# Optimization experiments

Measured on AMD Instinct MI355X. Metric: run time of the kernel, lower is better.

## Reference

```python
import jax, jax.numpy as jnp
import numpy as np

N_BUILDINGS = 4096
NUM_CLUSTERS = 128
EMBED_DIM = 128
TEMPORAL_DIM = 24


def setup_inputs() -> dict:
    key = jax.random.key(0)
    ks = jax.random.split(key, 12)
    E, N, C, T = EMBED_DIM, N_BUILDINGS, NUM_CLUSTERS, TEMPORAL_DIM

    def lin(k, fi, fo):
        k1, k2 = jax.random.split(k)
        w = jax.random.normal(k1, (fo, fi), jnp.float32) / np.sqrt(fi).astype(np.float32)
        b = jax.random.normal(k2, (fo,), jnp.float32) * 0.01
        return w, b

    fp_w1, fp_b1 = lin(ks[0], 2 * E + 2, 128)
    fp_w2, fp_b2 = lin(ks[1], 128, 64)
    fp_w3, fp_b3 = lin(ks[2], 64, 1)
    en_w1, en_b1 = lin(ks[3], 1, 16)
    en_w2, en_b2 = lin(ks[4], 16, 1)
    ps_w1, ps_b1 = lin(ks[5], E, 32)
    ps_w2, ps_b2 = lin(ks[6], 32, 1)

    embeddings = jax.random.normal(ks[7], (1, N, E), jnp.float32)
    generation = jax.random.uniform(ks[8], (1, N, T), jnp.float32) * 50.0
    consumption = jax.random.uniform(ks[9], (1, N, T), jnp.float32) * 50.0
    positions = jax.random.uniform(ks[10], (1, N, 2), jnp.float32) * 1000.0
    cluster_assignments = (jnp.arange(N) % C)[None, :].astype(jnp.int32)

    return dict(embeddings=embeddings, generation=generation, consumption=consumption,
                positions=positions,
                fp_w1=fp_w1, fp_b1=fp_b1, fp_w2=fp_w2, fp_b2=fp_b2, fp_w3=fp_w3, fp_b3=fp_b3,
                en_w1=en_w1, en_b1=en_b1, en_w2=en_w2, en_b2=en_b2,
                ps_w1=ps_w1, ps_b1=ps_b1, ps_w2=ps_w2, ps_b2=ps_b2,
                cluster_assignments=cluster_assignments, num_clusters=C, current_hour=12)


def _greedy_cluster(net0, prio, effm, pf):
    """Greedy allocation within one cluster. net0,prio: [K]; effm,pf: [K,K].
    Surplus rows and deficit cols are both visited in descending priority order;
    non-surplus rows have avail=0 and non-deficit cols have needed<=0, matching the
    original code's subset selection + break/continue semantics."""
    K = net0.shape[0]
    order = jnp.argsort(-prio)
    inv = jnp.argsort(order)
    net_o = net0[order]
    eff_o = effm[order][:, order]
    pf_o = pf[order][:, order]

    def outer(dnet, i):
        avail0 = jnp.maximum(net_o[i], 0.0)  # surplus net is never mutated

        def inner(carry, j):
            avail, dn = carry
            needed = -dn[j]
            active = (avail > 0.0) & (needed > 0.0)
            f = jnp.where(active, jnp.minimum(jnp.minimum(avail, needed), pf_o[i, j]), 0.0)
            dn = dn.at[j].add(f * eff_o[i, j])  # deficit receives delivered flow
            return (avail - f, dn), (f, active)

        (_, dnet), (frow, arow) = jax.lax.scan(inner, (avail0, dnet), jnp.arange(K))
        return dnet, (frow, arow)

    dnet, (flows_o, act_o) = jax.lax.scan(outer, net_o, jnp.arange(K))
    return flows_o[inv][:, inv], act_o[inv][:, inv], dnet[inv]


def _forward(embeddings, generation, consumption, positions,
             fp_w1, fp_b1, fp_w2, fp_b2, fp_w3, fp_b3,
             en_w1, en_b1, en_w2, en_b2,
             ps_w1, ps_b1, ps_w2, ps_b2,
             cluster_assignments, num_clusters, current_hour):
    B, N, E = embeddings.shape
    C = num_clusters
    K = N // C
    net = generation[0, :, current_hour] - consumption[0, :, current_hour]  # [N]

    g = jnp.argsort(cluster_assignments[0]).reshape(C, K)  # [C,K] building ids per cluster
    emb_c = embeddings[0][g]   # [C,K,E]
    pos_c = positions[0][g]    # [C,K,2]
    net_c = net[g]             # [C,K]

    # priority scorer (eval mode)
    h = jax.nn.relu(emb_c @ ps_w1.T + ps_b1)
    prio_c = jax.nn.sigmoid(h @ ps_w2.T + ps_b2)[..., 0]  # [C,K]

    # pairwise distances within cluster
    dist = jnp.linalg.norm(pos_c[:, :, None, :] - pos_c[:, None, :, :], axis=-1)  # [C,K,K]

    # efficiency net: eff = 0.85 + 0.13*sigmoid(MLP(dist/1000))
    eh = jax.nn.relu((dist / 1000.0)[..., None] * en_w1[:, 0] + en_b1)  # [C,K,K,16]
    eff = 0.85 + 0.13 * jax.nn.sigmoid(eh @ en_w2.T + en_b2)[..., 0]    # [C,K,K]

    # flow predictor on concat([emb_i, emb_j, dist, hour/24]); split W1 to avoid
    # materializing the [C,K,K,2E+2] feature tensor. Dropout is eval-mode identity.
    W1a, W1b = fp_w1[:, :E], fp_w1[:, E:2 * E]
    w1d, w1h = fp_w1[:, 2 * E], fp_w1[:, 2 * E + 1]
    hi = emb_c @ W1a.T  # [C,K,128]
    hj = emb_c @ W1b.T  # [C,K,128]
    hour_f = current_hour / 24.0
    h1 = jax.nn.relu(hi[:, :, None, :] + hj[:, None, :, :] + dist[..., None] * w1d + hour_f * w1h + fp_b1)
    h2 = jax.nn.relu(h1 @ fp_w2.T + fp_b2)
    pflow = jax.nn.softplus(h2 @ fp_w3.T + fp_b3)[..., 0]  # [C,K,K]

    flows_c, act_c, dnet_c = jax.vmap(_greedy_cluster)(net_c, prio_c, eff, pflow)

    sharing = jnp.zeros((N, N), embeddings.dtype).at[g[:, :, None], g[:, None, :]].set(flows_c)
    effmat = jnp.ones((N, N), embeddings.dtype).at[g[:, :, None], g[:, None, :]].set(
        jnp.where(act_c, eff, 1.0))
    net_after = jnp.zeros((N,), embeddings.dtype).at[g].set(dnet_c)

    sharing = sharing[None]
    effmat = effmat[None]
    total_shared = sharing.sum()
    energy_sent = sharing.sum(axis=2)
    energy_received = (sharing * effmat).sum(axis=1)
    return sharing, effmat, total_shared, energy_sent, energy_received, net_after[None]


def reference(embeddings, generation, consumption, positions,
              fp_w1, fp_b1, fp_w2, fp_b2, fp_w3, fp_b3,
              en_w1, en_b1, en_w2, en_b2,
              ps_w1, ps_b1, ps_w2, ps_b2,
              cluster_assignments, num_clusters, current_hour):
    return _forward(embeddings, generation, consumption, positions,
                    fp_w1, fp_b1, fp_w2, fp_b2, fp_w3, fp_b3,
                    en_w1, en_b1, en_w2, en_b2,
                    ps_w1, ps_b1, ps_w2, ps_b2,
                    cluster_assignments, num_clusters, current_hour)
```

## Files before the change

### kernel.cpp

```cpp
#include <hip/hip_runtime.h>
#include <math.h>

#define NB 4096
#define NC 128
#define NK 32
#define NE 128

typedef __bf16 bf16x8 __attribute__((ext_vector_type(8)));
typedef float floatx4 __attribute__((ext_vector_type(4)));

__device__ __forceinline__ float sigmoidf_(float x){
  if (x >= 0.f){ float z = expf(-x); return 1.f/(1.f+z); }
  float z = expf(x); return z/(1.f+z);
}
__device__ __forceinline__ float softplusf_(float x){
  return fmaxf(x, 0.f) + log1pf(expf(-fabsf(x)));
}
__device__ __forceinline__ unsigned int pack_bf16(float a, float b){
  unsigned short ua = __builtin_bit_cast(unsigned short, (__bf16)a);
  unsigned short ub = __builtin_bit_cast(unsigned short, (__bf16)b);
  return (unsigned int)ua | ((unsigned int)ub << 16);
}

__global__ void k_hijprio(const float* __restrict__ emb, const float* __restrict__ gen,
                          const float* __restrict__ cons, const float* __restrict__ fp_w1,
                          const float* __restrict__ fp_b1, const float* __restrict__ fp_w2,
                          const float* __restrict__ ps_w1, const float* __restrict__ ps_b1,
                          const float* __restrict__ ps_w2, const float* __restrict__ ps_b2,
                          const int* __restrict__ assign, const int* __restrict__ hourp,
                          float* __restrict__ hi, float* __restrict__ hj,
                          float* __restrict__ net, float* __restrict__ prio,
                          int* __restrict__ g, int* __restrict__ row_of,
                          float* __restrict__ w1d_c, float* __restrict__ bzc,
                          uint4* __restrict__ w2f, float* __restrict__ total){
  int bid = blockIdx.x;
  int t = threadIdx.x;
  if (bid < 512){
    __shared__ float es[8*132];
    __shared__ float wsm[32*132];
    __shared__ float wa_s[128*36];
    __shared__ float wb_s[128*36];
    int i0 = bid*8;
    for (int idx = t; idx < 8*128; idx += 256){
      int b = idx >> 7, e = idx & 127;
      es[b*132 + e] = emb[(i0 + b)*128 + e];
    }
    for (int idx = t; idx < 4096; idx += 256){
      int q = idx >> 7, e = idx & 127;
      wsm[q*132 + e] = ps_w1[q*128 + e];
    }
    int o = t & 127, half = t >> 7;
    float ai[4], aj[4];
#pragma unroll
    for (int r = 0; r < 4; ++r){ ai[r] = 0.f; aj[r] = 0.f; }
    for (int ch = 0; ch < 4; ++ch){
      int ec = ch << 5;
      if (ch) __syncthreads();
      for (int idx = t; idx < 4096; idx += 256){
        int row = idx >> 5, e2 = idx & 31;
        wa_s[row*36 + e2] = fp_w1[row*258 + ec + e2];
        wb_s[row*36 + e2] = fp_w1[row*258 + 128 + ec + e2];
      }
      __syncthreads();
      const float* war = &wa_s[o*36];
      const float* wbr = &wb_s[o*36];
#pragma unroll
      for (int e2 = 0; e2 < 32; e2 += 4){
        float4 wav = *(const float4*)&war[e2];
        float4 wbv = *(const float4*)&wbr[e2];
        float wa0 = wav.x, wa1 = wav.y, wa2 = wav.z, wa3 = wav.w;
        float wb0 = wbv.x, wb1 = wbv.y, wb2 = wbv.z, wb3 = wbv.w;
        int e = ec + e2;
#pragma unroll
        for (int r = 0; r < 4; ++r){
          float4 ev = *(const float4*)&es[(half*4 + r)*132 + e];
          ai[r] = fmaf(ev.x, wa0, fmaf(ev.y, wa1, fmaf(ev.z, wa2, fmaf(ev.w, wa3, ai[r]))));
          aj[r] = fmaf(ev.x, wb0, fmaf(ev.y, wb1, fmaf(ev.z, wb2, fmaf(ev.w, wb3, aj[r]))));
        }
      }
    }
#pragma unroll
    for (int r = 0; r < 4; ++r){
      int b = i0 + half*4 + r;
      hi[b*128 + o] = ai[r];
      hj[b*128 + o] = aj[r];
    }
    {
      int bl = t >> 5, q = t & 31;
      int i = i0 + bl;
      float acc = ps_b1[q];
      const float* er = &es[bl*132];
      const float* wr = &wsm[q*132];
      for (int e = 0; e < 128; e += 4){
        float4 ev = *(const float4*)&er[e];
        float4 wv = *(const float4*)&wr[e];
        acc = fmaf(ev.x, wv.x, acc);
        acc = fmaf(ev.y, wv.y, acc);
        acc = fmaf(ev.z, wv.z, acc);
        acc = fmaf(ev.w, wv.w, acc);
      }
      float v = fmaxf(acc, 0.f) * ps_w2[q];
      for (int m = 16; m >= 1; m >>= 1) v += __shfl_xor(v, m, 32);
      if (q == 0){
        prio[i] = sigmoidf_(v + ps_b2[0]);
        int h = hourp[0];
        net[i] = gen[i*24 + h] - cons[i*24 + h];
      }
    }
  } else if (bid < 528){
    __shared__ int hist[NC];
    __shared__ int loc[256];
    int start = (bid - 512)*256;
    for (int c = t; c < NC; c += 256) hist[c] = 0;
    __syncthreads();
    for (int j = t; j < start; j += 256) atomicAdd(&hist[assign[j]], 1);
    int i = start + t;
    int c = assign[i];
    loc[t] = c;
    __syncthreads();
    int r = hist[c];
    for (int j = 0; j < 256; ++j) r += (j < t && loc[j] == c) ? 1 : 0;
    if (r >= NK) r = NK - 1;
    g[c*NK + r] = i;
    row_of[i] = c*NK + r;
  } else if (bid == 528){
    if (t < 128){
      float hour_f = (float)hourp[0] / 24.0f;
      w1d_c[t] = fp_w1[t*258 + 256];
      bzc[t]   = fmaf(hour_f, fp_w1[t*258 + 257], fp_b1[t]);
    }
    if (t == 128) total[0] = 0.f;
  } else {
    for (int ff = t; ff < 1024; ff += 256){
      int lane = ff & 63, fi = ff >> 6;
      int nt = fi >> 2, ks = fi & 3;
      int o = nt*16 + (lane & 15);
      int kb = ks*32 + (lane >> 4)*8;
      const float* src = fp_w2 + o*128 + kb;
      uint4 u;
      u.x = pack_bf16(src[0], src[1]);
      u.y = pack_bf16(src[2], src[3]);
      u.z = pack_bf16(src[4], src[5]);
      u.w = pack_bf16(src[6], src[7]);
      w2f[ff] = u;
    }
  }
}

__global__ __launch_bounds__(512) void k_pflow(
    const float* __restrict__ hi, const float* __restrict__ hj,
    const float* __restrict__ pos, const float* __restrict__ w1d_c,
    const float* __restrict__ bzc, const uint4* __restrict__ w2f,
    const float* __restrict__ fp_b2, const float* __restrict__ fp_w3,
    const float* __restrict__ fp_b3, const float* __restrict__ en_w1,
    const float* __restrict__ en_b1, const float* __restrict__ en_w2,
    const float* __restrict__ en_b2, const int* __restrict__ g,
    float* __restrict__ pf_g, float* __restrict__ ef_g){
  __shared__ float px[32], py[32];
  __shared__ int gl[32];
  int t = threadIdx.x;
  int lane = t & 63, wv = t >> 6;
  int c = blockIdx.x >> 1, hb = blockIdx.x & 1;
  if (t < 32){
    int b = g[c*NK + t];
    gl[t] = b;
    px[t] = pos[2*b];
    py[t] = pos[2*b + 1];
  }
  __syncthreads();
  {
    int l16 = lane & 15, quad = lane >> 4;
    bf16x8 bfr[4][4];
#pragma unroll
    for (int nt = 0; nt < 4; ++nt)
#pragma unroll
      for (int ks = 0; ks < 4; ++ks)
        bfr[nt][ks] = __builtin_bit_cast(bf16x8, w2f[(nt*4 + ks)*64 + lane]);
    float b2v[4], w3v[4];
#pragma unroll
    for (int nt = 0; nt < 4; ++nt){
      b2v[nt] = fp_b2[nt*16 + l16];
      w3v[nt] = fp_w3[nt*16 + l16];
    }
    float b3 = fp_b3[0];
    const float4* wd4 = (const float4*)w1d_c;
    const float4* bz4 = (const float4*)bzc;
    for (int it = 0; it < 4; ++it){
      int tile = hb*32 + it*8 + wv;
      int i = tile >> 1, j0 = (tile & 1)*16;
      int j = j0 + l16;
      float dx = px[i] - px[j], dy = py[i] - py[j];
      float d = sqrtf(fmaf(dx, dx, dy*dy));
      const float4* hi4 = (const float4*)(hi + gl[i]*128);
      const float4* hj4 = (const float4*)(hj + gl[j]*128);
      bf16x8 af[4];
#pragma unroll
      for (int ks = 0; ks < 4; ++ks){
        int q8 = ks*8 + quad*2;
        float4 a0 = hi4[q8], a1 = hi4[q8 + 1];
        float4 b0 = hj4[q8], b1 = hj4[q8 + 1];
        float4 w0 = wd4[q8], w1 = wd4[q8 + 1];
        float4 z0 = bz4[q8], z1 = bz4[q8 + 1];
        float v0 = fmaxf(a0.x + b0.x + fmaf(d, w0.x, z0.x), 0.f);
        float v1 = fmaxf(a0.y + b0.y + fmaf(d, w0.y, z0.y), 0.f);
        float v2 = fmaxf(a0.z + b0.z + fmaf(d, w0.z, z0.z), 0.f);
        float v3 = fmaxf(a0.w + b0.w + fmaf(d, w0.w, z0.w), 0.f);
        float v4 = fmaxf(a1.x + b1.x + fmaf(d, w1.x, z1.x), 0.f);
        float v5 = fmaxf(a1.y + b1.y + fmaf(d, w1.y, z1.y), 0.f);
        float v6 = fmaxf(a1.z + b1.z + fmaf(d, w1.z, z1.z), 0.f);
        float v7 = fmaxf(a1.w + b1.w + fmaf(d, w1.w, z1.w), 0.f);
        uint4 u;
        u.x = pack_bf16(v0, v1);
        u.y = pack_bf16(v2, v3);
        u.z = pack_bf16(v4, v5);
        u.w = pack_bf16(v6, v7);
        af[ks] = __builtin_bit_cast(bf16x8, u);
      }
      floatx4 acc[4];
#pragma unroll
      for (int nt = 0; nt < 4; ++nt){
        acc[nt] = (floatx4){0.f, 0.f, 0.f, 0.f};
#pragma unroll
        for (int ks = 0; ks < 4; ++ks)
          acc[nt] = __builtin_amdgcn_mfma_f32_16x16x32_bf16(af[ks], bfr[nt][ks], acc[nt], 0, 0, 0);
      }
#pragma unroll
      for (int r = 0; r < 4; ++r){
        float s = 0.f;
#pragma unroll
        for (int nt = 0; nt < 4; ++nt)
          s = fmaf(fmaxf(acc[nt][r] + b2v[nt], 0.f), w3v[nt], s);
#pragma unroll
        for (int m = 8; m >= 1; m >>= 1) s += __shfl_xor(s, m);
        if (l16 == 0)
          pf_g[c*1024 + i*32 + j0 + quad*4 + r] = softplusf_(s + b3);
      }
    }
  }
  {
    int e = hb*512 + t;
    int ii = e >> 5, jj = e & 31;
    float dx = px[ii] - px[jj], dy = py[ii] - py[jj];
    float d = sqrtf(fmaf(dx, dx, dy*dy));
    float ds = d * (1.0f/1000.0f);
    float acc = en_b2[0];
#pragma unroll
    for (int q = 0; q < 16; ++q)
      acc = fmaf(fmaxf(fmaf(ds, en_w1[q], en_b1[q]), 0.f), en_w2[q], acc);
    ef_g[c*1024 + e] = 0.85f + 0.13f*sigmoidf_(acc);
  }
}

__global__ __launch_bounds__(256) void k_greedy(
    const float* __restrict__ net, const float* __restrict__ prio,
    const int* __restrict__ g, const float* __restrict__ pf_g,
    const float* __restrict__ ef_g,
    float* __restrict__ fl_c, float* __restrict__ ef_c, float* __restrict__ total,
    float* __restrict__ esent, float* __restrict__ erecv, float* __restrict__ nafter){
  __shared__ float pf_s[1024];
  __shared__ float ef_s[1024];
  __shared__ float fl_s[1024];
  __shared__ float efa_s[1024];
  __shared__ int gl[32];
  __shared__ int order_s[32];
  int t = threadIdx.x;
  int c = blockIdx.x;
  if (t < 32) gl[t] = g[c*NK + t];
  ((float4*)pf_s)[t] = ((const float4*)(pf_g + c*1024))[t];
  ((float4*)ef_s)[t] = ((const float4*)(ef_g + c*1024))[t];
  __syncthreads();
  if (t < 64){
    int tl = t & 31;
    float pr = (t < 32) ? prio[gl[t]] : -1e30f;
    int rank = 0;
    for (int k = 0; k < 32; ++k){
      float pk = __shfl(pr, k, 32);
      rank += ((pk > pr) || (pk == pr && k < tl)) ? 1 : 0;
    }
    if (t < 32) order_s[rank] = t;
  }
  __syncthreads();
  if (t < 64){
    int tl = t & 31;
    int b = order_s[tl];
    float net0 = net[gl[b]];
    float dnet = net0;
    float recv = 0.f;
    for (int i = 0; i < 32; ++i){
      int a = order_s[i];
      float av0 = fmaxf(__shfl(net0, i, 32), 0.f);
      float pf = pf_s[a*32 + b];
      float ef = ef_s[a*32 + b];
      float needed = -dnet;
      float m = (needed > 0.f) ? fminf(needed, pf) : 0.f;
      float s = m;
#pragma unroll
      for (int dd = 1; dd < 32; dd <<= 1){
        float u = __shfl_up(s, dd, 32);
        if (tl >= dd) s += u;
      }
      float Se = __shfl_up(s, 1, 32);
      if (tl == 0) Se = 0.f;
      float rprev = fmaxf(av0 - Se, 0.f);
      int act = (rprev > 0.f) && (needed > 0.f);
      float f = fminf(m, rprev);
      dnet = fmaf(f, ef, dnet);
      recv = fmaf(f, ef, recv);
      if (t < 32){
        fl_s[a*32 + b]  = f;
        efa_s[a*32 + b] = act ? ef : 1.0f;
      }
    }
    if (t < 32){
      nafter[gl[b]] = dnet;
      erecv[gl[b]]  = recv;
    }
  }
  __syncthreads();
  for (int e = t; e < 1024; e += 256){
    fl_c[c*1024 + e] = fl_s[e];
    ef_c[c*1024 + e] = efa_s[e];
  }
  if (t < 32){
    float rs = 0.f;
#pragma unroll
    for (int j = 0; j < 32; ++j)
      rs += fl_s[t*32 + ((j + t) & 31)];
    esent[gl[t]] = rs;
    float cs = rs;
    for (int m = 16; m >= 1; m >>= 1) cs += __shfl_xor(cs, m, 32);
    if (t == 0) atomicAdd(total, cs);
  }
}

__global__ __launch_bounds__(256) void k_write(
    const float* __restrict__ fl_c, const float* __restrict__ ef_c,
    const int* __restrict__ g, const int* __restrict__ row_of,
    float* __restrict__ sharing, float* __restrict__ effm){
  __shared__ float rowS[4096];
  __shared__ float rowE[4096];
  __shared__ int   cols[32];
  __shared__ float vals[32];
  __shared__ float vale[32];
  int t = threadIdx.x;
  int r = blockIdx.x;
  int ra = row_of[r];
  int c = ra >> 5, a = ra & 31;
  if (t < 32){
    cols[t] = g[c*NK + t];
    vals[t] = fl_c[c*1024 + a*32 + t];
    vale[t] = ef_c[c*1024 + a*32 + t];
  }
  float4 z4 = make_float4(0.f, 0.f, 0.f, 0.f);
  float4 o4 = make_float4(1.f, 1.f, 1.f, 1.f);
  float4* s4 = (float4*)rowS;
  float4* e4 = (float4*)rowE;
#pragma unroll
  for (int q = 0; q < 4; ++q){ s4[t + 256*q] = z4; e4[t + 256*q] = o4; }
  __syncthreads();
  if (t < 32){ rowS[cols[t]] = vals[t]; rowE[cols[t]] = vale[t]; }
  __syncthreads();
  const floatx4* s4v = (const floatx4*)rowS;
  const floatx4* e4v = (const floatx4*)rowE;
  floatx4* gs = (floatx4*)(sharing + (long)r*NB);
  floatx4* ge = (floatx4*)(effm    + (long)r*NB);
#pragma unroll
  for (int q = 0; q < 4; ++q){
    __builtin_nontemporal_store(s4v[t + 256*q], &gs[t + 256*q]);
    __builtin_nontemporal_store(e4v[t + 256*q], &ge[t + 256*q]);
  }
}

extern "C" void kernel_launch(void* const* d_in, const int* in_sizes, int n_in,
                              void* d_out, int out_size, void* d_ws, size_t ws_size,
                              hipStream_t stream){
  (void)in_sizes; (void)n_in; (void)out_size; (void)ws_size;
  const float* emb   = (const float*)d_in[0];
  const float* gen   = (const float*)d_in[1];
  const float* cons  = (const float*)d_in[2];
  const float* pos   = (const float*)d_in[3];
  const float* fp_w1 = (const float*)d_in[4];
  const float* fp_b1 = (const float*)d_in[5];
  const float* fp_w2 = (const float*)d_in[6];
  const float* fp_b2 = (const float*)d_in[7];
  const float* fp_w3 = (const float*)d_in[8];
  const float* fp_b3 = (const float*)d_in[9];
  const float* en_w1 = (const float*)d_in[10];
  const float* en_b1 = (const float*)d_in[11];
  const float* en_w2 = (const float*)d_in[12];
  const float* en_b2 = (const float*)d_in[13];
  const float* ps_w1 = (const float*)d_in[14];
  const float* ps_b1 = (const float*)d_in[15];
  const float* ps_w2 = (const float*)d_in[16];
  const float* ps_b2 = (const float*)d_in[17];
  const int*   assign = (const int*)d_in[18];
  const int*   hourp  = (const int*)d_in[20];

  char* ws = (char*)d_ws;
  int*   g      = (int*)  (ws + 0);
  int*   row_of = (int*)  (ws + 16384);
  float* net    = (float*)(ws + 32768);
  float* prio   = (float*)(ws + 49152);
  float* w1d_c  = (float*)(ws + 65536);
  float* bzc    = (float*)(ws + 66048);
  uint4* w2f    = (uint4*)(ws + 131072);
  float* hi     = (float*)(ws + 262144);
  float* hj     = (float*)(ws + 2359296);
  float* fl_c   = (float*)(ws + 4456448);
  float* ef_c   = (float*)(ws + 4980736);
  float* pf_g   = (float*)(ws + 5505024);
  float* ef_g   = (float*)(ws + 6029312);

  float* sharing = (float*)d_out;
  float* effm    = sharing + (long)NB*NB;
  float* total   = effm + (long)NB*NB;
  float* esent   = total + 1;
  float* erecv   = esent + NB;
  float* nafter  = erecv + NB;

  hipLaunchKernelGGL(k_hijprio, dim3(530), dim3(256), 0, stream,
                     emb, gen, cons, fp_w1, fp_b1, fp_w2, ps_w1, ps_b1, ps_w2, ps_b2,
                     assign, hourp, hi, hj, net, prio, g, row_of, w1d_c, bzc, w2f, total);
  hipLaunchKernelGGL(k_pflow, dim3(256), dim3(512), 0, stream,
                     hi, hj, pos, w1d_c, bzc, w2f, fp_b2, fp_w3, fp_b3,
                     en_w1, en_b1, en_w2, en_b2, g, pf_g, ef_g);
  hipLaunchKernelGGL(k_greedy, dim3(128), dim3(256), 0, stream,
                     net, prio, g, pf_g, ef_g,
                     fl_c, ef_c, total, esent, erecv, nafter);
  hipLaunchKernelGGL(k_write, dim3(4096), dim3(256), 0, stream,
                     fl_c, ef_c, g, row_of, sharing, effm);
}
```

Baseline: 247.4 us.

## Fuse greedy allocation with dense matrix write into a single kernel

Merges the greedy and dense-row writer kernels: each cluster is handled by two blocks that both redo the greedy pass, then each writes 16 full rows of the sharing and efficiency matrices directly, using a shared column-to-member lookup table. This drops the intermediate workspace round-trip and one kernel launch. The cost is that the greedy work is duplicated and only 256 blocks, each writing 16 rows serially, handle the 128 MB dense output instead of 4096 blocks, which may lower store parallelism.

```diff
diff --git a/kernel.cpp b/kernel.cpp
--- a/kernel.cpp
+++ b/kernel.cpp
@@ -251,24 +251,28 @@
   }
 }
 
-__global__ __launch_bounds__(256) void k_greedy(
+__global__ __launch_bounds__(256) void k_gw(
     const float* __restrict__ net, const float* __restrict__ prio,
     const int* __restrict__ g, const float* __restrict__ pf_g,
-    const float* __restrict__ ef_g,
-    float* __restrict__ fl_c, float* __restrict__ ef_c, float* __restrict__ total,
-    float* __restrict__ esent, float* __restrict__ erecv, float* __restrict__ nafter){
+    const float* __restrict__ ef_g, float* __restrict__ total,
+    float* __restrict__ esent, float* __restrict__ erecv, float* __restrict__ nafter,
+    float* __restrict__ sharing, float* __restrict__ effm){
   __shared__ float pf_s[1024];
   __shared__ float ef_s[1024];
   __shared__ float fl_s[1024];
   __shared__ float efa_s[1024];
-  __shared__ int gl[32];
-  __shared__ int order_s[32];
+  __shared__ int   mtbl[NB];
+  __shared__ int   gl[32];
+  __shared__ int   order_s[32];
   int t = threadIdx.x;
-  int c = blockIdx.x;
+  int c = blockIdx.x >> 1, hb = blockIdx.x & 1;
   if (t < 32) gl[t] = g[c*NK + t];
   ((float4*)pf_s)[t] = ((const float4*)(pf_g + c*1024))[t];
   ((float4*)ef_s)[t] = ((const float4*)(ef_g + c*1024))[t];
+#pragma unroll
+  for (int q = 0; q < 16; ++q) mtbl[q*256 + t] = -1;
   __syncthreads();
+  if (t < 32) mtbl[gl[t]] = t;
   if (t < 64){
     int tl = t & 31;
     float pr = (t < 32) ? prio[gl[t]] : -1e30f;
@@ -311,17 +315,13 @@
         efa_s[a*32 + b] = act ? ef : 1.0f;
       }
     }
-    if (t < 32){
+    if (hb == 0 && t < 32){
       nafter[gl[b]] = dnet;
       erecv[gl[b]]  = recv;
     }
   }
   __syncthreads();
-  for (int e = t; e < 1024; e += 256){
-    fl_c[c*1024 + e] = fl_s[e];
-    ef_c[c*1024 + e] = efa_s[e];
-  }
-  if (t < 32){
+  if (hb == 0 && t < 32){
     float rs = 0.f;
 #pragma unroll
     for (int j = 0; j < 32; ++j)
@@ -331,43 +331,31 @@
     for (int m = 16; m >= 1; m >>= 1) cs += __shfl_xor(cs, m, 32);
     if (t == 0) atomicAdd(total, cs);
   }
-}
-
-__global__ __launch_bounds__(256) void k_write(
-    const float* __restrict__ fl_c, const float* __restrict__ ef_c,
-    const int* __restrict__ g, const int* __restrict__ row_of,
-    float* __restrict__ sharing, float* __restrict__ effm){
-  __shared__ float rowS[4096];
-  __shared__ float rowE[4096];
-  __shared__ int   cols[32];
-  __shared__ float vals[32];
-  __shared__ float vale[32];
-  int t = threadIdx.x;
-  int r = blockIdx.x;
-  int ra = row_of[r];
-  int c = ra >> 5, a = ra & 31;
-  if (t < 32){
-    cols[t] = g[c*NK + t];
-    vals[t] = fl_c[c*1024 + a*32 + t];
-    vale[t] = ef_c[c*1024 + a*32 + t];
-  }
-  float4 z4 = make_float4(0.f, 0.f, 0.f, 0.f);
-  float4 o4 = make_float4(1.f, 1.f, 1.f, 1.f);
-  float4* s4 = (float4*)rowS;
-  float4* e4 = (float4*)rowE;
-#pragma unroll
-  for (int q = 0; q < 4; ++q){ s4[t + 256*q] = z4; e4[t + 256*q] = o4; }
-  __syncthreads();
-  if (t < 32){ rowS[cols[t]] = vals[t]; rowE[cols[t]] = vale[t]; }
-  __syncthreads();
-  const floatx4* s4v = (const floatx4*)rowS;
-  const floatx4* e4v = (const floatx4*)rowE;
-  floatx4* gs = (floatx4*)(sharing + (long)r*NB);
-  floatx4* ge = (floatx4*)(effm    + (long)r*NB);
-#pragma unroll
-  for (int q = 0; q < 4; ++q){
-    __builtin_nontemporal_store(s4v[t + 256*q], &gs[t + 256*q]);
-    __builtin_nontemporal_store(e4v[t + 256*q], &ge[t + 256*q]);
+  int mjq[16];
+#pragma unroll
+  for (int q = 0; q < 4; ++q)
+#pragma unroll
+    for (int x = 0; x < 4; ++x)
+      mjq[q*4 + x] = mtbl[q*1024 + t*4 + x];
+  for (int al = 0; al < 16; ++al){
+    int a = hb*16 + al;
+    long row = (long)gl[a] * NB;
+    const float* flr = &fl_s[a*32];
+    const float* efr = &efa_s[a*32];
+    floatx4* gs = (floatx4*)(sharing + row);
+    floatx4* ge = (floatx4*)(effm + row);
+#pragma unroll
+    for (int q = 0; q < 4; ++q){
+      floatx4 vs = (floatx4){0.f, 0.f, 0.f, 0.f};
+      floatx4 ve = (floatx4){1.f, 1.f, 1.f, 1.f};
+#pragma unroll
+      for (int x = 0; x < 4; ++x){
+        int mj = mjq[q*4 + x];
+        if (mj >= 0){ vs[x] = flr[mj]; ve[x] = efr[mj]; }
+      }
+      __builtin_nontemporal_store(vs, &gs[q*256 + t]);
+      __builtin_nontemporal_store(ve, &ge[q*256 + t]);
+    }
   }
 }
 
@@ -406,8 +394,6 @@
   uint4* w2f    = (uint4*)(ws + 131072);
   float* hi     = (float*)(ws + 262144);
   float* hj     = (float*)(ws + 2359296);
-  float* fl_c   = (float*)(ws + 4456448);
-  float* ef_c   = (float*)(ws + 4980736);
   float* pf_g   = (float*)(ws + 5505024);
   float* ef_g   = (float*)(ws + 6029312);
 
@@ -424,9 +410,7 @@
   hipLaunchKernelGGL(k_pflow, dim3(256), dim3(512), 0, stream,
                      hi, hj, pos, w1d_c, bzc, w2f, fp_b2, fp_w3, fp_b3,
                      en_w1, en_b1, en_w2, en_b2, g, pf_g, ef_g);
-  hipLaunchKernelGGL(k_greedy, dim3(128), dim3(256), 0, stream,
-                     net, prio, g, pf_g, ef_g,
-                     fl_c, ef_c, total, esent, erecv, nafter);
-  hipLaunchKernelGGL(k_write, dim3(4096), dim3(256), 0, stream,
-                     fl_c, ef_c, g, row_of, sharing, effm);
-}
+  hipLaunchKernelGGL(k_gw, dim3(256), dim3(256), 0, stream,
+                     net, prio, g, pf_g, ef_g, total, esent, erecv, nafter,
+                     sharing, effm);
+}
```

New measurement: 241.3 us, median of 2. -2.5%, faster.
